# Kernel tuning notes

Hardware: AMD Instinct MI355X
Metric: run time of the kernel (lower is better)

The kernel has to match this reference:

```python
import jax, jax.numpy as jnp
import numpy as np

N, D, B, O, E = 4096, 1024, 512, 1, 16  # samples, in_size, bottleneck, out_size, n_tasks
L1_LAMBDA = 1e-4


def setup_inputs() -> dict:
    key = jax.random.key(0)
    ks = jax.random.split(key, 6)
    x = jax.random.normal(ks[0], (N, D), jnp.float32)
    keys = jax.random.randint(ks[1], (N,), 0, E, dtype=jnp.int32)
    W1 = jax.random.normal(ks[2], (E, B, D), jnp.float32) / np.sqrt(D).astype(np.float32)
    b1 = jax.random.normal(ks[3], (E, B), jnp.float32) * 0.01
    W2 = jax.random.normal(ks[4], (E, O, B), jnp.float32) / np.sqrt(B).astype(np.float32)
    b2 = jax.random.normal(ks[5], (E, O), jnp.float32) * 0.01
    return {"x": x, "keys": keys, "W1": W1, "b1": b1, "W2": W2, "b2": b2}


def reference(x, keys, W1, b1, W2, b2):
    """Per-sample task-specific 2-layer bottleneck MLP dispatch.

    x: [N, D] float; keys: [N] int task indices.
    W1: [E, B, D], b1: [E, B], W2: [E, O, B], b2: [E, O].
    Returns (out [N, O], l1_lambda * sum_n L1(params of expert keys[n])).
    """
    n = x.shape[0]
    e = W1.shape[0]
    # Dense MoE dispatch: first linear for all experts, then select per sample.
    h_all = jnp.einsum('nd,ebd->neb', x, W1) + b1[None]          # [N, E, B]
    h = h_all[jnp.arange(n), keys]                                # [N, B]
    h = jax.nn.relu(h)                                            # activation='relu'
    out = jnp.einsum('nb,nob->no', h, W2[keys]) + b2[keys]        # [N, O]
    # L1 of the selected expert's parameters is accumulated once per sample.
    l1_per_expert = (jnp.abs(W1).sum((1, 2)) + jnp.abs(b1).sum(1)
                     + jnp.abs(W2).sum((1, 2)) + jnp.abs(b2).sum(1))  # [E]
    counts = jnp.zeros((e,), x.dtype).at[keys].add(jnp.ones((), x.dtype))
    l1 = jnp.asarray(L1_LAMBDA, x.dtype) * jnp.dot(counts, l1_per_expert)
    return out, l1
```

## Files before the change

### kernel.cpp

```cpp
#include <hip/hip_runtime.h>
#include <hip/hip_bf16.h>

#define N_S 4096
#define D_IN 1024
#define B_BOT 512
#define E_EXP 16
#define L1_LAMBDA 1e-4f

#define MT 64
#define NT 128
#define KC 64
#define MT_GRID 6
#define IDSTR 512

typedef float f32x4 __attribute__((ext_vector_type(4)));
typedef short bf16x8 __attribute__((ext_vector_type(8)));
typedef unsigned int u32;


__device__ __forceinline__ ushort4 cvt4(float4 v) {
    union { __hip_bfloat162 b2[2]; ushort4 u4; } u;
    u.b2[0] = __float22bfloat162_rn({v.x, v.y});
    u.b2[1] = __float22bfloat162_rn({v.z, v.w});
    return u.u4;
}

__device__ __forceinline__ void async16(const ushort* g, ushort* l) {
    __builtin_amdgcn_global_load_lds(
        (const __attribute__((address_space(1))) u32*)g,
        (__attribute__((address_space(3))) u32*)l, 16, 0, 0);
}

__global__ __launch_bounds__(256)
void prep_kernel(const float* __restrict__ x, const int* __restrict__ keys,
                 const float* __restrict__ W1, const float* __restrict__ b1,
                 const float* __restrict__ W2, const float* __restrict__ b2,
                 float* __restrict__ out, int* __restrict__ counts,
                 float* __restrict__ l1small, float* __restrict__ l1part,
                 int* __restrict__ ids, ushort* __restrict__ W1b,
                 ushort* __restrict__ xb) {
    const int blk = blockIdx.x;
    const int t = threadIdx.x;
    if (blk < E_EXP) {
        const int e = blk;
        out[e * 256 + t] = 0.f;
        float s = fabsf(b1[e * B_BOT + t]) + fabsf(b1[e * B_BOT + 256 + t])
                + fabsf(W2[e * B_BOT + t]) + fabsf(W2[e * B_BOT + 256 + t]);
        if (t == 0) s += fabsf(b2[e]);
#pragma unroll
        for (int off = 32; off > 0; off >>= 1) s += __shfl_down(s, off);
        __shared__ float ws4a[4];
        __shared__ int cnt_s;
        if ((t & 63) == 0) ws4a[t >> 6] = s;
        if (t == 0) cnt_s = 0;
        __syncthreads();
        if (t == 0) l1small[e] = ws4a[0] + ws4a[1] + ws4a[2] + ws4a[3];
        const int lane = t & 63;
        for (int it = 0; it < N_S / 256; ++it) {
            const int i = it * 256 + t;
            const bool m = (keys[i] == e);
            const unsigned long long mask = __ballot(m);
            int base = 0;
            if (lane == 0) base = atomicAdd(&cnt_s, __popcll(mask));
            base = __shfl(base, 0);
            if (m) {
                const int pos = base + __popcll(mask & ((1ull << lane) - 1ull));
                if (pos < IDSTR) ids[e * IDSTR + pos] = i;
            }
        }
        __syncthreads();
        if (t == 0) counts[e] = min(cnt_s, IDSTR);
    } else if (blk < E_EXP + 1024) {
        const int i = blk - E_EXP;
        const int g = i & 7, h = i >> 3;
        const int e = g + 8 * (h & 1);
        const int sub = h >> 1;
        const long long base = (long long)e * 131072 + (long long)sub * 2048;
        const float4* __restrict__ src = (const float4*)W1;
        ushort4* __restrict__ dst = (ushort4*)W1b;
        float s = 0.f;
#pragma unroll
        for (int m = 0; m < 8; ++m) {
            const long long idx = base + m * 256 + t;
            float4 v = src[idx];
            s += fabsf(v.x) + fabsf(v.y) + fabsf(v.z) + fabsf(v.w);
            dst[idx] = cvt4(v);
        }
#pragma unroll
        for (int off = 32; off > 0; off >>= 1) s += __shfl_down(s, off);
        __shared__ float ws4b[4];
        if ((t & 63) == 0) ws4b[t >> 6] = s;
        __syncthreads();
        if (t == 0) l1part[e * 64 + sub] = ws4b[0] + ws4b[1] + ws4b[2] + ws4b[3];
    } else {
        const int i = blk - E_EXP - 1024;
        const long long base = (long long)i * 2048;
        const float4* __restrict__ src = (const float4*)x;
        ushort4* __restrict__ dst = (ushort4*)xb;
#pragma unroll
        for (int m = 0; m < 8; ++m) {
            const long long idx = base + m * 256 + t;
            dst[idx] = cvt4(src[idx]);
        }
    }
}

__global__ __launch_bounds__(256, 2)
void mlp_kernel(const ushort* __restrict__ W1b, const ushort* __restrict__ xb,
                const float* __restrict__ b1, const float* __restrict__ W2,
                const float* __restrict__ b2, const int* __restrict__ counts,
                const float* __restrict__ l1small, const float* __restrict__ l1part,
                const int* __restrict__ ids, float* __restrict__ out) {
    const int b = blockIdx.x;
    const int mt = b >> 6, nb = (b >> 4) & 3, e = b & 15;
    const int t = threadIdx.x, wave = t >> 6, lane = t & 63;
    const int l15 = lane & 15, qd = lane >> 4;
    const int wm = wave & 1, wn = wave >> 1;

    __shared__ __align__(16) ushort As0[MT * KC];
    __shared__ __align__(16) ushort As1[MT * KC];
    __shared__ __align__(16) ushort Bs0[NT * KC];
    __shared__ __align__(16) ushort Bs1[NT * KC];
    __shared__ int sid_s[MT];
    __shared__ float red[2][MT];

    if (b == 0 && wave == 0) {
        const int el = lane >> 2, sub = lane & 3;
        float s = 0.f;
#pragma unroll
        for (int k = 0; k < 16; ++k) s += l1part[el * 64 + sub * 16 + k];
        s += __shfl_xor(s, 1);
        s += __shfl_xor(s, 2);
        float v = (sub == 0) ? (float)counts[el] * (s + l1small[el]) : 0.f;
        v += __shfl_xor(v, 4);
        v += __shfl_xor(v, 8);
        v += __shfl_xor(v, 16);
        v += __shfl_xor(v, 32);
        if (lane == 0) out[N_S] = L1_LAMBDA * v;
    }

    const int cnt = counts[e];
    const int m0 = mt * MT;
    if (m0 >= cnt) return;

    if (t < MT) sid_s[t] = ids[e * IDSTR + min(m0 + t, cnt - 1)];
    __syncthreads();

    const int colb = nb * NT;
    float b1v[4], w2v[4];
#pragma unroll
    for (int j = 0; j < 4; ++j) {
        const int col = colb + 64 * wn + 16 * j + l15;
        b1v[j] = b1[e * B_BOT + col];
        w2v[j] = W2[e * B_BOT + col];
    }
    const float b2e = b2[e];

    const ushort* gA[2];
    const int dldsA[2] = {(0 * 256 + wave * 64) * 8, (1 * 256 + wave * 64) * 8};
#pragma unroll
    for (int p = 0; p < 2; ++p) {
        const int u = p * 256 + t, r = u >> 3;
        const int q = (u & 7) ^ (r & 7);
        gA[p] = xb + (size_t)sid_s[r] * D_IN + q * 8;
    }
    const ushort* gB[4];
    int dldsB[4];
#pragma unroll
    for (int p = 0; p < 4; ++p) {
        const int u = p * 256 + t, r = u >> 3;
        const int q = (u & 7) ^ (r & 7);
        gB[p] = W1b + (size_t)(e * B_BOT + colb + r) * D_IN + q * 8;
        dldsB[p] = (p * 256 + wave * 64) * 8;
    }

    int offA[2][2], offB[4][2];
#pragma unroll
    for (int i = 0; i < 2; ++i)
#pragma unroll
        for (int s = 0; s < 2; ++s) {
            const int r = 32 * wm + 16 * i + l15;
            offA[i][s] = (r * 8 + ((s * 4 + qd) ^ (r & 7))) * 8;
        }
#pragma unroll
    for (int j = 0; j < 4; ++j)
#pragma unroll
        for (int s = 0; s < 2; ++s) {
            const int r = 64 * wn + 16 * j + l15;
            offB[j][s] = (r * 8 + ((s * 4 + qd) ^ (r & 7))) * 8;
        }

    f32x4 acc[2][4];
#pragma unroll
    for (int i = 0; i < 2; ++i)
#pragma unroll
        for (int j = 0; j < 4; ++j) acc[i][j] = (f32x4){0.f, 0.f, 0.f, 0.f};

#define STAGE(ko, Ad, Bd)                                         \
    do {                                                          \
        _Pragma("unroll")                                         \
        for (int p = 0; p < 2; ++p)                               \
            async16(gA[p] + (ko), (Ad) + dldsA[p]);               \
        _Pragma("unroll")                                         \
        for (int p = 0; p < 4; ++p)                               \
            async16(gB[p] + (ko), (Bd) + dldsB[p]);               \
    } while (0)

#define COMPUTE(Ab, Bb)                                                        \
    do {                                                                       \
        _Pragma("unroll")                                                      \
        for (int s = 0; s < 2; ++s) {                                          \
            bf16x8 a0 = *(const bf16x8*)((Ab) + offA[0][s]);                   \
            bf16x8 a1 = *(const bf16x8*)((Ab) + offA[1][s]);                   \
            bf16x8 bb[4];                                                      \
            _Pragma("unroll")                                                  \
            for (int j = 0; j < 4; ++j)                                        \
                bb[j] = *(const bf16x8*)((Bb) + offB[j][s]);                   \
            _Pragma("unroll")                                                  \
            for (int j = 0; j < 4; ++j) {                                      \
                acc[0][j] = __builtin_amdgcn_mfma_f32_16x16x32_bf16(           \
                    a0, bb[j], acc[0][j], 0, 0, 0);                            \
                acc[1][j] = __builtin_amdgcn_mfma_f32_16x16x32_bf16(           \
                    a1, bb[j], acc[1][j], 0, 0, 0);                            \
            }                                                                  \
        }                                                                      \
    } while (0)

    STAGE(0, As0, Bs0);
    __syncthreads();

#pragma unroll 1
    for (int c = 0; c < D_IN / KC; c += 2) {
        if (c + 1 < D_IN / KC) STAGE((c + 1) * KC, As1, Bs1);
        COMPUTE(As0, Bs0);
        __syncthreads();
        if (c + 2 < D_IN / KC) STAGE((c + 2) * KC, As0, Bs0);
        COMPUTE(As1, Bs1);
        __syncthreads();
    }
#undef STAGE
#undef COMPUTE

    float p[2][4] = {{0.f, 0.f, 0.f, 0.f}, {0.f, 0.f, 0.f, 0.f}};
#pragma unroll
    for (int j = 0; j < 4; ++j)
#pragma unroll
        for (int i = 0; i < 2; ++i)
#pragma unroll
            for (int r = 0; r < 4; ++r) {
                const float h = fmaxf(acc[i][j][r] + b1v[j], 0.f);
                p[i][r] = fmaf(h, w2v[j], p[i][r]);
            }
#pragma unroll
    for (int off = 8; off > 0; off >>= 1)
#pragma unroll
        for (int i = 0; i < 2; ++i)
#pragma unroll
            for (int r = 0; r < 4; ++r) p[i][r] += __shfl_xor(p[i][r], off, 16);

    if (l15 == 0) {
#pragma unroll
        for (int i = 0; i < 2; ++i)
#pragma unroll
            for (int r = 0; r < 4; ++r)
                red[wn][32 * wm + 16 * i + 4 * qd + r] = p[i][r];
    }
    __syncthreads();
    if (t < MT) {
        const int m = m0 + t;
        if (m < cnt) {
            float v = red[0][t] + red[1][t];
            if (nb == 0) v += b2e;
            atomicAdd(&out[ids[e * IDSTR + m]], v);
        }
    }
}

extern "C" void kernel_launch(void* const* d_in, const int* in_sizes, int n_in,
                              void* d_out, int out_size, void* d_ws, size_t ws_size,
                              hipStream_t stream) {
    const float* x    = (const float*)d_in[0];
    const int*   keys = (const int*)d_in[1];
    const float* W1   = (const float*)d_in[2];
    const float* b1   = (const float*)d_in[3];
    const float* W2   = (const float*)d_in[4];
    const float* b2   = (const float*)d_in[5];
    float* out = (float*)d_out;

    char* ws = (char*)d_ws;
    int*    counts  = (int*)(ws + 0);
    float*  l1small = (float*)(ws + 64);
    float*  l1part  = (float*)(ws + 128);
    int*    ids     = (int*)(ws + 4224);
    ushort* W1b     = (ushort*)(ws + 65536);
    ushort* xb      = (ushort*)(ws + 65536 + 16777216);

    prep_kernel<<<E_EXP + 1024 + 512, 256, 0, stream>>>(
        x, keys, W1, b1, W2, b2, out, counts, l1small, l1part, ids, W1b, xb);
    mlp_kernel<<<MT_GRID * 64, 256, 0, stream>>>(
        W1b, xb, b1, W2, b2, counts, l1small, l1part, ids, out);
}
```

Baseline: 112.5 us.

## Triple-buffer LDS tiles with vmcnt-based waits and one barrier per chunk

Replaces the double-buffered K loop with a three-stage LDS ring that keeps two chunks of async global-to-LDS loads in flight. Each iteration waits with s_waitcnt vmcnt(6) only for the oldest chunk, then issues a single barrier, instead of draining every load and synchronising twice per pair of chunks. This aims to hide more memory latency behind the MFMA work. It raises LDS use per block by half, which could limit occupancy, and it depends on exact counting of outstanding loads.

```diff
diff --git a/kernel.cpp b/kernel.cpp
--- a/kernel.cpp
+++ b/kernel.cpp
@@ -10,6 +10,7 @@
 #define MT 64
 #define NT 128
 #define KC 64
+#define NCH (D_IN / KC)
 #define MT_GRID 6
 #define IDSTR 512
 
@@ -117,10 +118,8 @@
     const int l15 = lane & 15, qd = lane >> 4;
     const int wm = wave & 1, wn = wave >> 1;
 
-    __shared__ __align__(16) ushort As0[MT * KC];
-    __shared__ __align__(16) ushort As1[MT * KC];
-    __shared__ __align__(16) ushort Bs0[NT * KC];
-    __shared__ __align__(16) ushort Bs1[NT * KC];
+    __shared__ __align__(16) ushort As[3][MT * KC];
+    __shared__ __align__(16) ushort Bs[3][NT * KC];
     __shared__ int sid_s[MT];
     __shared__ float red[2][MT];
 
@@ -196,26 +195,30 @@
 #pragma unroll
         for (int j = 0; j < 4; ++j) acc[i][j] = (f32x4){0.f, 0.f, 0.f, 0.f};
 
-#define STAGE(ko, Ad, Bd)                                         \
+#define STAGE(ko, bi)                                             \
     do {                                                          \
+        ushort* Ad = &As[bi][0];                                  \
+        ushort* Bd = &Bs[bi][0];                                  \
         _Pragma("unroll")                                         \
         for (int p = 0; p < 2; ++p)                               \
-            async16(gA[p] + (ko), (Ad) + dldsA[p]);               \
+            async16(gA[p] + (ko), Ad + dldsA[p]);                 \
         _Pragma("unroll")                                         \
         for (int p = 0; p < 4; ++p)                               \
-            async16(gB[p] + (ko), (Bd) + dldsB[p]);               \
+            async16(gB[p] + (ko), Bd + dldsB[p]);                 \
     } while (0)
 
-#define COMPUTE(Ab, Bb)                                                        \
+#define COMPUTE(bi)                                                            \
     do {                                                                       \
+        const ushort* Ab = &As[bi][0];                                         \
+        const ushort* Bb = &Bs[bi][0];                                         \
         _Pragma("unroll")                                                      \
         for (int s = 0; s < 2; ++s) {                                          \
-            bf16x8 a0 = *(const bf16x8*)((Ab) + offA[0][s]);                   \
-            bf16x8 a1 = *(const bf16x8*)((Ab) + offA[1][s]);                   \
+            bf16x8 a0 = *(const bf16x8*)(Ab + offA[0][s]);                     \
+            bf16x8 a1 = *(const bf16x8*)(Ab + offA[1][s]);                     \
             bf16x8 bb[4];                                                      \
             _Pragma("unroll")                                                  \
             for (int j = 0; j < 4; ++j)                                        \
-                bb[j] = *(const bf16x8*)((Bb) + offB[j][s]);                   \
+                bb[j] = *(const bf16x8*)(Bb + offB[j][s]);                     \
             _Pragma("unroll")                                                  \
             for (int j = 0; j < 4; ++j) {                                      \
                 acc[0][j] = __builtin_amdgcn_mfma_f32_16x16x32_bf16(           \
@@ -226,17 +229,26 @@
         }                                                                      \
     } while (0)
 
-    STAGE(0, As0, Bs0);
-    __syncthreads();
-
+    STAGE(0, 0);
+    STAGE(KC, 1);
+
+    int cur = 0, nxt2 = 2;
 #pragma unroll 1
-    for (int c = 0; c < D_IN / KC; c += 2) {
-        if (c + 1 < D_IN / KC) STAGE((c + 1) * KC, As1, Bs1);
-        COMPUTE(As0, Bs0);
-        __syncthreads();
-        if (c + 2 < D_IN / KC) STAGE((c + 2) * KC, As0, Bs0);
-        COMPUTE(As1, Bs1);
-        __syncthreads();
+    for (int c = 0; c < NCH; ++c) {
+        if (c + 2 < NCH) {
+            asm volatile("s_waitcnt vmcnt(6)" ::: "memory");
+            __builtin_amdgcn_s_barrier();
+            STAGE((c + 2) * KC, nxt2);
+        } else if (c + 1 < NCH) {
+            asm volatile("s_waitcnt vmcnt(6)" ::: "memory");
+            __builtin_amdgcn_s_barrier();
+        } else {
+            asm volatile("s_waitcnt vmcnt(0)" ::: "memory");
+            __builtin_amdgcn_s_barrier();
+        }
+        COMPUTE(cur);
+        cur = (cur == 2) ? 0 : cur + 1;
+        nxt2 = (nxt2 == 2) ? 0 : nxt2 + 1;
     }
 #undef STAGE
 #undef COMPUTE
```

New measurement: 115.2 us. 2.4% more time.
